# Optimization experiments

Measured on AMD Instinct MI355X. Metric: run time of the kernel, lower is better.

## Reference

```python
import jax, jax.numpy as jnp
import numpy as np

EMBED = 1024
ADIM = 1024
H = 16
HD = ADIM // H          # 64
RAY = 48                # ray_subdim
R = RAY // 3            # 16
SCALE = 1.0 / np.sqrt(HD)
NB = 768                # boundary tokens
MN = 8                  # max neighbors
FG = 6                  # face_group
L = 1024                # tokens per face
B = 12                  # b * face_group
STAGES = 4


def _apply_dray(x, d, einsum_str, inverse):
    ray = x[..., :RAY].reshape(x.shape[:-1] + (3, R))
    if inverse:
        d = jnp.swapaxes(d, -1, -2)
    ray = jnp.einsum(einsum_str, d, ray).reshape(x.shape[:-1] + (RAY,))
    return jnp.concatenate([ray, x[..., RAY:]], axis=-1)


def setup_inputs() -> dict:
    key = jax.random.key(0)
    ks = jax.random.split(key, 12)
    inp = {}
    inp['x'] = jax.random.normal(ks[0], (B, L, EMBED), dtype=jnp.float32)
    inp['qkv_w'] = jax.random.normal(ks[1], (EMBED, 3 * ADIM), dtype=jnp.float32) * 0.02
    inp['out_w'] = jax.random.normal(ks[2], (ADIM, EMBED), dtype=jnp.float32) * 0.02
    inp['out_b'] = jax.random.normal(ks[3], (EMBED,), dtype=jnp.float32) * 0.02
    inp['d_ray'] = jax.random.normal(ks[4], (STAGES, FG, L, 3, 3), dtype=jnp.float32)
    inp['boundary_face_ids'] = jax.random.randint(ks[5], (NB,), 0, FG, dtype=jnp.int32).astype(jnp.int64)
    inp['boundary_token_indices'] = jnp.arange(NB, dtype=jnp.int64)
    inp['boundary_local_indices'] = jax.random.randint(ks[6], (NB,), 0, L, dtype=jnp.int32).astype(jnp.int64)
    inp['boundary_stage_ids'] = jax.random.randint(ks[7], (NB,), 0, STAGES, dtype=jnp.int32).astype(jnp.int64)
    inp['neighbor_face_ids'] = jax.random.randint(ks[8], (NB, MN), 0, FG, dtype=jnp.int32).astype(jnp.int64)
    inp['neighbor_token_indices'] = jax.random.randint(ks[9], (NB, MN), 0, L, dtype=jnp.int32).astype(jnp.int64)
    inp['neighbor_local_indices'] = jax.random.randint(ks[10], (NB, MN), 0, L, dtype=jnp.int32).astype(jnp.int64)
    inp['neighbor_stage_ids'] = jax.random.randint(ks[11], (NB, MN), 0, STAGES, dtype=jnp.int32).astype(jnp.int64)
    inp['neighbor_mask'] = jnp.ones((NB, MN), dtype=bool)
    inp['face_group'] = FG
    return inp


def reference(x, qkv_w, out_w, out_b, d_ray,
              boundary_face_ids, boundary_token_indices, boundary_local_indices, boundary_stage_ids,
              neighbor_face_ids, neighbor_token_indices, neighbor_local_indices, neighbor_stage_ids,
              neighbor_mask, face_group):
    b = x.shape[0] // face_group
    l = x.shape[1]
    xt = x.reshape(b, face_group, l, EMBED)          # [b, FG, L, E]
    max_face, max_idx = face_group - 1, l - 1

    qf = jnp.clip(boundary_face_ids, 0, max_face)
    qi = jnp.clip(boundary_token_indices, 0, max_idx)
    valid_q = (boundary_face_ids == qf) & (boundary_token_indices == qi)

    nf = jnp.clip(neighbor_face_ids, 0, max_face)
    ni = jnp.clip(neighbor_token_indices, 0, max_idx)
    mask = neighbor_mask & (neighbor_face_ids == nf) & (neighbor_token_indices == ni)

    # gather boundary queries and neighbor keys/values
    x_q = xt[:, qf, qi, :]                            # [b, NB, E]
    x_kv = xt[:, nf, ni, :]                           # [b, NB, MN, E]
    q = (x_q @ qkv_w)[..., :ADIM]
    kv = x_kv @ qkv_w
    k = kv[..., ADIM:2 * ADIM]
    v = kv[..., 2 * ADIM:]

    nb, mn = q.shape[1], k.shape[2]
    q = q.reshape(b, nb, H, HD)
    k = k.reshape(b, nb, mn, H, HD)
    v = v.reshape(b, nb, mn, H, HD)

    d_q = d_ray[boundary_stage_ids, boundary_face_ids, boundary_local_indices]     # [NB, 3, 3]
    d_k = d_ray[neighbor_stage_ids,
                jnp.maximum(neighbor_face_ids, 0),
                jnp.maximum(neighbor_local_indices, 0)]                            # [NB, MN, 3, 3]

    q = _apply_dray(q, d_q, 'nij,bnhjr->bnhir', inverse=False)
    k = _apply_dray(k, d_k, 'nmij,bnmhjr->bnmhir', inverse=False)
    v = _apply_dray(v, d_k, 'nmij,bnmhjr->bnmhir', inverse=False)

    attn = jnp.einsum('bnhd,bnmhd->bnmh', q, k) * SCALE
    attn = jnp.where(mask[None, :, :, None], attn, -jnp.inf)
    attn = jax.nn.softmax(attn, axis=2)               # softmax over neighbors
    out = jnp.einsum('bnmh,bnmhd->bnhd', attn, v)

    out = _apply_dray(out, d_q, 'nij,bnhjr->bnhir', inverse=True)
    out = out.reshape(b, nb, ADIM) @ out_w + out_b
    out = out * valid_q[None, :, None].astype(out.dtype)

    out_full = jnp.zeros_like(xt).at[:, qf, qi, :].set(out)
    return out_full.reshape(-1, l, EMBED)
```

## Files before the change

kernel.cpp:

```cpp
#include <hip/hip_runtime.h>
#include <hip/hip_bf16.h>
#include <cstddef>

#define FG 6
#define L 1024
#define NB 768
#define MN 8
#define H 16
#define HD 64
#define ADIM 1024
#define STAGES 4
#define SCALE 0.125f

typedef __attribute__((ext_vector_type(8))) short bf16x8;
typedef __attribute__((ext_vector_type(4))) float f32x4;
typedef __attribute__((address_space(3))) short lds_short_t;
typedef const __attribute__((address_space(1))) short g_short_t;

__device__ __forceinline__ int clampi(int v, int lo, int hi) {
  return v < lo ? lo : (v > hi ? hi : v);
}

__device__ __forceinline__ short f2bf(float f) {
  __hip_bfloat16 h = __float2bfloat16(f);
  return *reinterpret_cast<short*>(&h);
}

__device__ __forceinline__ float bf2f(short s) {
  __hip_bfloat16 h = *reinterpret_cast<__hip_bfloat16*>(&s);
  return __bfloat162float(h);
}

__device__ __forceinline__ void gload16(const short* g, short* l) {
  __builtin_amdgcn_global_load_lds((g_short_t*)g, (lds_short_t*)l, 16, 0, 0);
}

__global__ __launch_bounds__(256)
void prep_kernel(const float* __restrict__ x, short* __restrict__ xb,
                 float* __restrict__ zout,
                 const float* __restrict__ qkv_w, short* __restrict__ qwT,
                 const float* __restrict__ out_w, short* __restrict__ owT) {
  const int b = blockIdx.x;
  if (b < 12288) {
    const size_t zi = ((size_t)b * 256 + threadIdx.x) * 4;
    *(float4*)(zout + zi) = (float4){0.f, 0.f, 0.f, 0.f};
    if (b >= 6144) return;
    size_t i = ((size_t)b * 256 + threadIdx.x) * 8;
    float4 a = *(const float4*)(x + i);
    float4 c = *(const float4*)(x + i + 4);
    bf16x8 v;
    v[0] = f2bf(a.x); v[1] = f2bf(a.y); v[2] = f2bf(a.z); v[3] = f2bf(a.w);
    v[4] = f2bf(c.x); v[5] = f2bf(c.y); v[6] = f2bf(c.z); v[7] = f2bf(c.w);
    *(bf16x8*)(xb + i) = v;
    return;
  }
  int t = b - 12288;
  const float* in; short* out; int N, n0, k0;
  if (t < 3072) { in = qkv_w; out = qwT; N = 3072; n0 = (t % 96) * 32; k0 = (t / 96) * 32; }
  else { t -= 3072; in = out_w; out = owT; N = 1024; n0 = (t % 32) * 32; k0 = (t / 32) * 32; }
  __shared__ float tile[32][33];
  const int tx = threadIdx.x & 31, ty = threadIdx.x >> 5;
  #pragma unroll
  for (int i = 0; i < 4; ++i)
    tile[ty + i * 8][tx] = in[(size_t)(k0 + ty + i * 8) * N + n0 + tx];
  __syncthreads();
  #pragma unroll
  for (int i = 0; i < 4; ++i)
    out[(size_t)(n0 + ty + i * 8) * 1024 + k0 + tx] =
        f2bf(tile[tx][ty + i * 8]);
}

__global__ __launch_bounds__(256)
void q_gemm64(const short* __restrict__ A, const short* __restrict__ B,
              float* __restrict__ C,
              const int* __restrict__ f_ids, const int* __restrict__ t_ids)
{
  __shared__ __align__(16) short As[4096];
  __shared__ __align__(16) short Bs[8192];

  const int tid = threadIdx.x;
  const int w = tid >> 6, lane = tid & 63;
  const int row0 = blockIdx.y * 64, col0 = blockIdx.x * 128;
  const int lr = lane & 15, lq = lane >> 4;
  const int wrow = (w >> 1) * 32, wcol = (w & 1) * 64;

  size_t asrc[2]; short* adst[2];
  #pragma unroll
  for (int c = 0; c < 2; ++c) {
    const int d = c * 256 + tid, r = d >> 3;
    const int ss = (d & 7) ^ (r & 7);
    const int rr = row0 + r;
    const int bi = rr >= NB;
    const int idx = rr - bi * NB;
    const int f = clampi(f_ids[idx], 0, FG - 1);
    const int q = clampi(t_ids[idx], 0, L - 1);
    asrc[c] = (size_t)((bi * FG + f) * L + q) * 1024 + ss * 8;
    adst[c] = As + d * 8;
  }
  size_t bsrc[4]; short* bdst[4];
  #pragma unroll
  for (int c = 0; c < 4; ++c) {
    const int d = c * 256 + tid, r = d >> 3;
    const int ss = (d & 7) ^ (r & 7);
    bsrc[c] = (size_t)(col0 + r) * 1024 + ss * 8;
    bdst[c] = Bs + d * 8;
  }

  const char* As8 = (const char*)As;
  const char* Bs8 = (const char*)Bs;
  const int swz = lr & 7;

  f32x4 acc[2][4];
  #pragma unroll
  for (int m = 0; m < 2; ++m)
    #pragma unroll
    for (int n = 0; n < 4; ++n) acc[m][n] = (f32x4){0.f, 0.f, 0.f, 0.f};

  for (int kt = 0; kt < 16; ++kt) {
    #pragma unroll
    for (int c = 0; c < 2; ++c) gload16(A + asrc[c] + kt * 64, adst[c]);
    #pragma unroll
    for (int c = 0; c < 4; ++c) gload16(B + bsrc[c] + kt * 64, bdst[c]);
    __syncthreads();
    #pragma unroll
    for (int kk = 0; kk < 2; ++kk) {
      const int so = ((kk * 4 + lq) ^ swz) << 4;
      bf16x8 av[2], bv[4];
      #pragma unroll
      for (int m = 0; m < 2; ++m)
        av[m] = *(const bf16x8*)(As8 + (wrow + m * 16 + lr) * 128 + so);
      #pragma unroll
      for (int n = 0; n < 4; ++n)
        bv[n] = *(const bf16x8*)(Bs8 + (wcol + n * 16 + lr) * 128 + so);
      #pragma unroll
      for (int m = 0; m < 2; ++m)
        #pragma unroll
        for (int n = 0; n < 4; ++n)
          acc[m][n] = __builtin_amdgcn_mfma_f32_16x16x32_bf16(
              av[m], bv[n], acc[m][n], 0, 0, 0);
    }
    __syncthreads();
  }

  #pragma unroll
  for (int m = 0; m < 2; ++m)
    #pragma unroll
    for (int j = 0; j < 4; ++j) {
      const int r = row0 + wrow + m * 16 + lq * 4 + j;
      #pragma unroll
      for (int n = 0; n < 4; ++n)
        C[(size_t)r * 1024 + col0 + wcol + n * 16 + lr] = acc[m][n][j];
    }
}


#define BAR()   do { __builtin_amdgcn_s_barrier(); __builtin_amdgcn_sched_barrier(0); } while (0)
#define LGKM(N) do { asm volatile("s_waitcnt lgkmcnt(" #N ")" ::: "memory"); __builtin_amdgcn_sched_barrier(0); } while (0)
#define VMC(N)  do { asm volatile("s_waitcnt vmcnt(" #N ")" ::: "memory"); __builtin_amdgcn_sched_barrier(0); } while (0)
#define PRIO1   __builtin_amdgcn_s_setprio(1)
#define PRIO0   __builtin_amdgcn_s_setprio(0)

#define LDA6(D, FB, KK, BUF)                                                  \
  { _Pragma("unroll")                                                         \
    for (int f_ = 0; f_ < 3; ++f_) {                                          \
      const int row_ = (2 * ((FB) + f_) + wm) * 16 + lr;                      \
      D[f_] = *(const bf16x8*)(As8 + (BUF) * 24576 + row_ * 128               \
               + ((((KK) * 4 + lq) ^ swz) << 4));                             \
    } }

#define LDB4(D, KK, BUF)                                                      \
  { _Pragma("unroll")                                                         \
    for (int g_ = 0; g_ < 4; ++g_) {                                          \
      const int row_ = wn * 64 + g_ * 16 + lr;                                \
      D[g_] = *(const bf16x8*)(Bs8 + (BUF) * 32768 + row_ * 128               \
               + ((((KK) * 4 + lq) ^ swz) << 4));                             \
    } }

#define MM6(AV, BV, FB)                                                       \
  { _Pragma("unroll")                                                         \
    for (int f_ = 0; f_ < 3; ++f_)                                            \
      _Pragma("unroll")                                                       \
      for (int g_ = 0; g_ < 4; ++g_)                                          \
        acc[(FB) + f_][g_] = __builtin_amdgcn_mfma_f32_16x16x32_bf16(         \
            AV[f_], BV[g_], acc[(FB) + f_][g_], 0, 0, 0); }

__global__ __launch_bounds__(512, 2)
void kv_gemm192(const short* __restrict__ A, const short* __restrict__ B,
                short* __restrict__ C,
                const int* __restrict__ f_ids, const int* __restrict__ t_ids)
{
  __shared__ __align__(16) short As[24576];
  __shared__ __align__(16) short Bs[32768];

  const int tid = threadIdx.x;
  const int w = tid >> 6, lane = tid & 63;
  const int wm = w >> 2, wn = w & 3;
  const int lr = lane & 15, lq = lane >> 4;
  const int row0 = blockIdx.y * 192;
  const int col0 = blockIdx.x * 256;

  const int ssrc = (((tid & 7) ^ ((tid >> 3) & 7))) * 8;

  size_t a_src[3];
  #pragma unroll
  for (int c = 0; c < 3; ++c) {
    const int rr = row0 + c * 64 + (tid >> 3);
    const int bi = rr >= NB * MN;
    const int idx = rr - bi * (NB * MN);
    const int f = clampi(f_ids[idx], 0, FG - 1);
    const int q = clampi(t_ids[idx], 0, L - 1);
    a_src[c] = (size_t)((bi * FG + f) * L + q) * 1024 + ssrc;
  }
  size_t b_src[2][2];
  #pragma unroll
  for (int h = 0; h < 2; ++h)
    #pragma unroll
    for (int i = 0; i < 2; ++i)
      b_src[h][i] = (size_t)(1024 + col0 + h * 128 + ((tid + i * 512) >> 3)) * 1024 + ssrc;

  auto stgA = [&](int c, int kt, int buf) {
    gload16(A + a_src[c] + kt * 64, As + buf * 12288 + c * 4096 + tid * 8);
  };
  auto stgB = [&](int h, int kt, int buf) {
    gload16(B + b_src[h][0] + kt * 64, Bs + buf * 16384 + h * 8192 + tid * 8);
    gload16(B + b_src[h][1] + kt * 64, Bs + buf * 16384 + h * 8192 + 4096 + tid * 8);
  };

  const char* As8 = (const char*)As;
  const char* Bs8 = (const char*)Bs;
  const int swz = lane & 7;

  f32x4 acc[6][4];
  #pragma unroll
  for (int f = 0; f < 6; ++f)
    #pragma unroll
    for (int g = 0; g < 4; ++g) acc[f][g] = (f32x4){0.f, 0.f, 0.f, 0.f};

  bf16x8 avA[3], avB[3], bv0[4], bv1[4];

  stgB(0, 0, 0); stgB(1, 0, 0); stgA(0, 0, 0); stgA(1, 0, 0); stgA(2, 0, 0);
  stgB(0, 1, 1); stgB(1, 1, 1); stgA(0, 1, 1);
  VMC(5); BAR();

  for (int I = 0; I < 7; ++I) {
    const int kA = 2 * I + 1, kB = 2 * I + 2, kC = 2 * I + 3;
    LDA6(avA, 0, 0, 0); LDB4(bv0, 0, 0); LDA6(avB, 0, 1, 0); LDB4(bv1, 1, 0);
    stgA(1, kA, 1); stgA(2, kA, 1);
    BAR(); LGKM(0); PRIO1; MM6(avA, bv0, 0); MM6(avB, bv1, 0); PRIO0; BAR();
    LDA6(avA, 3, 0, 0); LDA6(avB, 3, 1, 0);
    stgB(0, kB, 0); stgB(1, kB, 0); stgA(0, kB, 0);
    BAR(); LGKM(0); PRIO1; MM6(avA, bv0, 3); MM6(avB, bv1, 3); PRIO0; VMC(5); BAR();
    LDA6(avA, 0, 0, 1); LDB4(bv0, 0, 1); LDA6(avB, 0, 1, 1); LDB4(bv1, 1, 1);
    stgA(1, kB, 0); stgA(2, kB, 0);
    BAR(); LGKM(0); PRIO1; MM6(avA, bv0, 0); MM6(avB, bv1, 0); PRIO0; BAR();
    LDA6(avA, 3, 0, 1); LDA6(avB, 3, 1, 1);
    stgB(0, kC, 1); stgB(1, kC, 1); stgA(0, kC, 1);
    BAR(); LGKM(0); PRIO1; MM6(avA, bv0, 3); MM6(avB, bv1, 3); PRIO0; VMC(5); BAR();
  }

  {
    LDA6(avA, 0, 0, 0); LDB4(bv0, 0, 0); LDA6(avB, 0, 1, 0); LDB4(bv1, 1, 0);
    stgA(1, 15, 1); stgA(2, 15, 1);
    BAR(); LGKM(0); PRIO1; MM6(avA, bv0, 0); MM6(avB, bv1, 0); PRIO0; BAR();

    LDA6(avA, 3, 0, 0); LDA6(avB, 3, 1, 0);
    BAR(); LGKM(0); PRIO1; MM6(avA, bv0, 3); MM6(avB, bv1, 3); PRIO0; VMC(0); BAR();

    LDA6(avA, 0, 0, 1); LDB4(bv0, 0, 1); LDA6(avB, 0, 1, 1); LDB4(bv1, 1, 1);
    BAR(); LGKM(0); PRIO1; MM6(avA, bv0, 0); MM6(avB, bv1, 0); PRIO0; BAR();

    LDA6(avA, 3, 0, 1); LDA6(avB, 3, 1, 1);
    BAR(); LGKM(0); PRIO1; MM6(avA, bv0, 3); MM6(avB, bv1, 3); PRIO0;
  }

  #pragma unroll
  for (int f = 0; f < 6; ++f) {
    #pragma unroll
    for (int j = 0; j < 4; ++j) {
      const int r = row0 + (2 * f + wm) * 16 + lq * 4 + j;
      short* cp = C + (size_t)r * 2048 + col0 + wn * 64 + lr;
      #pragma unroll
      for (int g = 0; g < 4; ++g)
        cp[g * 16] = f2bf(acc[f][g][j]);
    }
  }
}

__global__ __launch_bounds__(256)
void out_gemm64(const short* __restrict__ A, const short* __restrict__ B,
                float* __restrict__ C,
                const int* __restrict__ f_ids, const int* __restrict__ t_ids,
                const float* __restrict__ bias)
{
  __shared__ __align__(16) short As[4096];
  __shared__ __align__(16) short Bs[8192];

  const int tid = threadIdx.x;
  const int w = tid >> 6, lane = tid & 63;
  const int row0 = blockIdx.y * 64, col0 = blockIdx.x * 128;
  const int lr = lane & 15, lq = lane >> 4;
  const int wrow = (w >> 1) * 32, wcol = (w & 1) * 64;

  size_t asrc[2]; short* adst[2];
  #pragma unroll
  for (int c = 0; c < 2; ++c) {
    const int d = c * 256 + tid, r = d >> 3;
    const int ss = (d & 7) ^ (r & 7);
    asrc[c] = (size_t)(row0 + r) * 1024 + ss * 8;
    adst[c] = As + d * 8;
  }
  size_t bsrc[4]; short* bdst[4];
  #pragma unroll
  for (int c = 0; c < 4; ++c) {
    const int d = c * 256 + tid, r = d >> 3;
    const int ss = (d & 7) ^ (r & 7);
    bsrc[c] = (size_t)(col0 + r) * 1024 + ss * 8;
    bdst[c] = Bs + d * 8;
  }

  const char* As8 = (const char*)As;
  const char* Bs8 = (const char*)Bs;
  const int swz = lr & 7;

  f32x4 acc[2][4];
  #pragma unroll
  for (int m = 0; m < 2; ++m)
    #pragma unroll
    for (int n = 0; n < 4; ++n) acc[m][n] = (f32x4){0.f, 0.f, 0.f, 0.f};

  for (int kt = 0; kt < 16; ++kt) {
    #pragma unroll
    for (int c = 0; c < 2; ++c) gload16(A + asrc[c] + kt * 64, adst[c]);
    #pragma unroll
    for (int c = 0; c < 4; ++c) gload16(B + bsrc[c] + kt * 64, bdst[c]);
    __syncthreads();
    #pragma unroll
    for (int kk = 0; kk < 2; ++kk) {
      const int so = ((kk * 4 + lq) ^ swz) << 4;
      bf16x8 av[2], bv[4];
      #pragma unroll
      for (int m = 0; m < 2; ++m)
        av[m] = *(const bf16x8*)(As8 + (wrow + m * 16 + lr) * 128 + so);
      #pragma unroll
      for (int n = 0; n < 4; ++n)
        bv[n] = *(const bf16x8*)(Bs8 + (wcol + n * 16 + lr) * 128 + so);
      #pragma unroll
      for (int m = 0; m < 2; ++m)
        #pragma unroll
        for (int n = 0; n < 4; ++n)
          acc[m][n] = __builtin_amdgcn_mfma_f32_16x16x32_bf16(
              av[m], bv[n], acc[m][n], 0, 0, 0);
    }
    __syncthreads();
  }

  float bb[4];
  #pragma unroll
  for (int n = 0; n < 4; ++n) bb[n] = bias[col0 + wcol + n * 16 + lr];
  #pragma unroll
  for (int m = 0; m < 2; ++m)
    #pragma unroll
    for (int j = 0; j < 4; ++j) {
      const int r  = row0 + wrow + m * 16 + lq * 4 + j;
      const int bi = r >= NB;
      const int nn = r - bi * NB;
      const int bf = f_ids[nn], bt = t_ids[nn];
      const int qf = clampi(bf, 0, FG - 1), qi = clampi(bt, 0, L - 1);
      const bool valid = (bf == qf) && (bt == qi);
      const size_t obase = ((size_t)(bi * FG + qf) * L + qi) * 1024;
      #pragma unroll
      for (int n = 0; n < 4; ++n) {
        const int col = col0 + wcol + n * 16 + lr;
        C[obase + col] = valid ? (acc[m][n][j] + bb[n]) : 0.f;
      }
    }
}

__global__ __launch_bounds__(256)
void attn_kernel2(const float* __restrict__ dray,
                  const int* __restrict__ bfid, const int* __restrict__ blid,
                  const int* __restrict__ bsid,
                  const int* __restrict__ nfid, const int* __restrict__ ntid,
                  const int* __restrict__ nlid, const int* __restrict__ nsid,
                  const int* __restrict__ nmask,
                  const float* __restrict__ qbuf,
                  const short* __restrict__ kvbuf,
                  __hip_bfloat16* __restrict__ obuf)
{
  __shared__ __align__(16) short kvlds[MN * 2048];
  __shared__ float smdq[9];
  __shared__ float smdk[MN][9];
  __shared__ int   smok[MN];

  const int bn   = blockIdx.x;
  const int n    = bn % NB;
  const int tid  = threadIdx.x;
  const int w    = tid >> 6, lane = tid & 63;

  const short* kvb = kvbuf + (size_t)bn * MN * 2048;
  #pragma unroll
  for (int j = 0; j < 8; ++j)
    gload16(kvb + (j * 256 + tid) * 8, kvlds + (j * 256 + tid) * 8);

  if (tid < 9) {
    int st = clampi(bsid[n], 0, STAGES - 1);
    int f  = clampi(bfid[n], 0, FG - 1);
    int lc = clampi(blid[n], 0, L - 1);
    smdq[tid] = dray[((size_t)(st * FG + f) * L + lc) * 9 + tid];
  } else if (tid >= 64 && tid < 136) {
    const int t = tid - 64, m = t / 9, j = t - m * 9;
    const int idx = n * MN + m;
    int nst = clampi(nsid[idx], 0, STAGES - 1);
    int nfc = clampi(nfid[idx], 0, FG - 1);
    int nlc = clampi(nlid[idx], 0, L - 1);
    smdk[m][j] = dray[((size_t)(nst * FG + nfc) * L + nlc) * 9 + j];
  } else if (tid >= 192 && tid < 192 + MN) {
    const int m = tid - 192;
    const int idx = n * MN + m;
    int nf = nfid[idx], nt = ntid[idx];
    smok[m] = (nmask[idx] != 0) && nf >= 0 && nf < FG && nt >= 0 && nt < L;
  }
  __syncthreads();

  float dq[9];
  #pragma unroll
  for (int t = 0; t < 9; ++t) dq[t] = smdq[t];

  const int rr = lane & 15;

  for (int hi = 0; hi < 4; ++hi) {
    const int h = hi * 4 + w;

    const float qraw = qbuf[(size_t)bn * ADIM + h * HD + lane];
    float x0 = __shfl(qraw, rr), x1 = __shfl(qraw, 16 + rr), x2 = __shfl(qraw, 32 + rr);
    float q0 = dq[0]*x0 + dq[1]*x1 + dq[2]*x2;
    float q1 = dq[3]*x0 + dq[4]*x1 + dq[5]*x2;
    float q2 = dq[6]*x0 + dq[7]*x1 + dq[8]*x2;
    float qd = lane < 16 ? q0 : lane < 32 ? q1 : lane < 48 ? q2 : qraw;

    float s[MN], vd[MN];
    #pragma unroll
    for (int m = 0; m < MN; ++m) {
      float dk[9];
      #pragma unroll
      for (int t = 0; t < 9; ++t) dk[t] = smdk[m][t];

      float kraw = bf2f(kvlds[m * 2048 + h * HD + lane]);
      float k0 = __shfl(kraw, rr), k1 = __shfl(kraw, 16 + rr), k2 = __shfl(kraw, 32 + rr);
      float kr0 = dk[0]*k0 + dk[1]*k1 + dk[2]*k2;
      float kr1 = dk[3]*k0 + dk[4]*k1 + dk[5]*k2;
      float kr2 = dk[6]*k0 + dk[7]*k1 + dk[8]*k2;
      float kd = lane < 16 ? kr0 : lane < 32 ? kr1 : lane < 48 ? kr2 : kraw;

      float p = qd * kd;
      #pragma unroll
      for (int off = 32; off; off >>= 1) p += __shfl_xor(p, off);
      s[m] = p;

      float vraw = bf2f(kvlds[m * 2048 + 1024 + h * HD + lane]);
      float v0 = __shfl(vraw, rr), v1 = __shfl(vraw, 16 + rr), v2 = __shfl(vraw, 32 + rr);
      float vr0 = dk[0]*v0 + dk[1]*v1 + dk[2]*v2;
      float vr1 = dk[3]*v0 + dk[4]*v1 + dk[5]*v2;
      float vr2 = dk[6]*v0 + dk[7]*v1 + dk[8]*v2;
      vd[m] = lane < 16 ? vr0 : lane < 32 ? vr1 : lane < 48 ? vr2 : vraw;
    }

    float mx = -INFINITY;
    #pragma unroll
    for (int m = 0; m < MN; ++m) {
      s[m] = smok[m] ? s[m] * SCALE : -INFINITY;
      mx = fmaxf(mx, s[m]);
    }
    float den = 0.f;
    #pragma unroll
    for (int m = 0; m < MN; ++m) { s[m] = expf(s[m] - mx); den += s[m]; }
    float inv = 1.0f / den;

    float od = 0.f;
    #pragma unroll
    for (int m = 0; m < MN; ++m) od += s[m] * vd[m];
    od *= inv;

    float y0 = __shfl(od, rr), y1 = __shfl(od, 16 + rr), y2 = __shfl(od, 32 + rr);
    float t0 = dq[0]*y0 + dq[3]*y1 + dq[6]*y2;
    float t1 = dq[1]*y0 + dq[4]*y1 + dq[7]*y2;
    float t2 = dq[2]*y0 + dq[5]*y1 + dq[8]*y2;
    float outd = lane < 16 ? t0 : lane < 32 ? t1 : lane < 48 ? t2 : od;

    obuf[(size_t)bn * ADIM + h * HD + lane] = __float2bfloat16(outd);
  }
}

extern "C" void kernel_launch(void* const* d_in, const int* in_sizes, int n_in,
                              void* d_out, int out_size, void* d_ws, size_t ws_size,
                              hipStream_t stream) {
  const float* x     = (const float*)d_in[0];
  const float* qkv_w = (const float*)d_in[1];
  const float* out_w = (const float*)d_in[2];
  const float* out_b = (const float*)d_in[3];
  const float* dray  = (const float*)d_in[4];
  const int* bfid  = (const int*)d_in[5];
  const int* btid  = (const int*)d_in[6];
  const int* blid  = (const int*)d_in[7];
  const int* bsid  = (const int*)d_in[8];
  const int* nfid  = (const int*)d_in[9];
  const int* ntid  = (const int*)d_in[10];
  const int* nlid  = (const int*)d_in[11];
  const int* nsid  = (const int*)d_in[12];
  const int* nmask = (const int*)d_in[13];

  char* ws = (char*)d_ws;
  short* xb    = (short*)(ws);
  short* qwT   = (short*)(ws + 25165824);
  short* owT   = (short*)(ws + 31457280);
  float* qbuf  = (float*)(ws + 33554432);
  short* kvbuf = (short*)(ws + 39845888);
  short* obuf  = (short*)(ws + 90177536);

  prep_kernel<<<16384, 256, 0, stream>>>(x, xb, (float*)d_out,
                                         qkv_w, qwT, out_w, owT);

  q_gemm64<<<dim3(8, 24), 256, 0, stream>>>(xb, qwT, qbuf, bfid, btid);
  kv_gemm192<<<dim3(8, 64), 512, 0, stream>>>(xb, qwT, kvbuf, nfid, ntid);
  attn_kernel2<<<1536, 256, 0, stream>>>(dray, bfid, blid, bsid,
                                         nfid, ntid, nlid, nsid, nmask,
                                         qbuf, kvbuf,
                                         (__hip_bfloat16*)obuf);
  out_gemm64<<<dim3(8, 24), 256, 0, stream>>>(obuf, owT, (float*)d_out,
                                              bfid, btid, out_b);
}
```

Measured before the change: 154.8 us.

## Fuse Q projection GEMM into KV GEMM kernel as a second pass

```diff
diff --git a/kernel.cpp b/kernel.cpp
--- a/kernel.cpp
+++ b/kernel.cpp
@@ -70,90 +70,6 @@
         f2bf(tile[tx][ty + i * 8]);
 }
 
-__global__ __launch_bounds__(256)
-void q_gemm64(const short* __restrict__ A, const short* __restrict__ B,
-              float* __restrict__ C,
-              const int* __restrict__ f_ids, const int* __restrict__ t_ids)
-{
-  __shared__ __align__(16) short As[4096];
-  __shared__ __align__(16) short Bs[8192];
-
-  const int tid = threadIdx.x;
-  const int w = tid >> 6, lane = tid & 63;
-  const int row0 = blockIdx.y * 64, col0 = blockIdx.x * 128;
-  const int lr = lane & 15, lq = lane >> 4;
-  const int wrow = (w >> 1) * 32, wcol = (w & 1) * 64;
-
-  size_t asrc[2]; short* adst[2];
-  #pragma unroll
-  for (int c = 0; c < 2; ++c) {
-    const int d = c * 256 + tid, r = d >> 3;
-    const int ss = (d & 7) ^ (r & 7);
-    const int rr = row0 + r;
-    const int bi = rr >= NB;
-    const int idx = rr - bi * NB;
-    const int f = clampi(f_ids[idx], 0, FG - 1);
-    const int q = clampi(t_ids[idx], 0, L - 1);
-    asrc[c] = (size_t)((bi * FG + f) * L + q) * 1024 + ss * 8;
-    adst[c] = As + d * 8;
-  }
-  size_t bsrc[4]; short* bdst[4];
-  #pragma unroll
-  for (int c = 0; c < 4; ++c) {
-    const int d = c * 256 + tid, r = d >> 3;
-    const int ss = (d & 7) ^ (r & 7);
-    bsrc[c] = (size_t)(col0 + r) * 1024 + ss * 8;
-    bdst[c] = Bs + d * 8;
-  }
-
-  const char* As8 = (const char*)As;
-  const char* Bs8 = (const char*)Bs;
-  const int swz = lr & 7;
-
-  f32x4 acc[2][4];
-  #pragma unroll
-  for (int m = 0; m < 2; ++m)
-    #pragma unroll
-    for (int n = 0; n < 4; ++n) acc[m][n] = (f32x4){0.f, 0.f, 0.f, 0.f};
-
-  for (int kt = 0; kt < 16; ++kt) {
-    #pragma unroll
-    for (int c = 0; c < 2; ++c) gload16(A + asrc[c] + kt * 64, adst[c]);
-    #pragma unroll
-    for (int c = 0; c < 4; ++c) gload16(B + bsrc[c] + kt * 64, bdst[c]);
-    __syncthreads();
-    #pragma unroll
-    for (int kk = 0; kk < 2; ++kk) {
-      const int so = ((kk * 4 + lq) ^ swz) << 4;
-      bf16x8 av[2], bv[4];
-      #pragma unroll
-      for (int m = 0; m < 2; ++m)
-        av[m] = *(const bf16x8*)(As8 + (wrow + m * 16 + lr) * 128 + so);
-      #pragma unroll
-      for (int n = 0; n < 4; ++n)
-        bv[n] = *(const bf16x8*)(Bs8 + (wcol + n * 16 + lr) * 128 + so);
-      #pragma unroll
-      for (int m = 0; m < 2; ++m)
-        #pragma unroll
-        for (int n = 0; n < 4; ++n)
-          acc[m][n] = __builtin_amdgcn_mfma_f32_16x16x32_bf16(
-              av[m], bv[n], acc[m][n], 0, 0, 0);
-    }
-    __syncthreads();
-  }
-
-  #pragma unroll
-  for (int m = 0; m < 2; ++m)
-    #pragma unroll
-    for (int j = 0; j < 4; ++j) {
-      const int r = row0 + wrow + m * 16 + lq * 4 + j;
-      #pragma unroll
-      for (int n = 0; n < 4; ++n)
-        C[(size_t)r * 1024 + col0 + wcol + n * 16 + lr] = acc[m][n][j];
-    }
-}
-
-
 #define BAR()   do { __builtin_amdgcn_s_barrier(); __builtin_amdgcn_sched_barrier(0); } while (0)
 #define LGKM(N) do { asm volatile("s_waitcnt lgkmcnt(" #N ")" ::: "memory"); __builtin_amdgcn_sched_barrier(0); } while (0)
 #define VMC(N)  do { asm volatile("s_waitcnt vmcnt(" #N ")" ::: "memory"); __builtin_amdgcn_sched_barrier(0); } while (0)
@@ -184,20 +100,16 @@
         acc[(FB) + f_][g_] = __builtin_amdgcn_mfma_f32_16x16x32_bf16(         \
             AV[f_], BV[g_], acc[(FB) + f_][g_], 0, 0, 0); }
 
-__global__ __launch_bounds__(512, 2)
-void kv_gemm192(const short* __restrict__ A, const short* __restrict__ B,
-                short* __restrict__ C,
-                const int* __restrict__ f_ids, const int* __restrict__ t_ids)
+__device__ __forceinline__ void gemm192_pass(
+    const short* __restrict__ A, const short* __restrict__ B,
+    int row0, int col0, int bcol0, int MROW,
+    const int* __restrict__ f_ids, const int* __restrict__ t_ids,
+    short* As, short* Bs, f32x4 (&acc)[6][4])
 {
-  __shared__ __align__(16) short As[24576];
-  __shared__ __align__(16) short Bs[32768];
-
   const int tid = threadIdx.x;
   const int w = tid >> 6, lane = tid & 63;
   const int wm = w >> 2, wn = w & 3;
   const int lr = lane & 15, lq = lane >> 4;
-  const int row0 = blockIdx.y * 192;
-  const int col0 = blockIdx.x * 256;
 
   const int ssrc = (((tid & 7) ^ ((tid >> 3) & 7))) * 8;
 
@@ -205,8 +117,8 @@
   #pragma unroll
   for (int c = 0; c < 3; ++c) {
     const int rr = row0 + c * 64 + (tid >> 3);
-    const int bi = rr >= NB * MN;
-    const int idx = rr - bi * (NB * MN);
+    const int bi = rr >= MROW;
+    const int idx = rr - bi * MROW;
     const int f = clampi(f_ids[idx], 0, FG - 1);
     const int q = clampi(t_ids[idx], 0, L - 1);
     a_src[c] = (size_t)((bi * FG + f) * L + q) * 1024 + ssrc;
@@ -216,7 +128,7 @@
   for (int h = 0; h < 2; ++h)
     #pragma unroll
     for (int i = 0; i < 2; ++i)
-      b_src[h][i] = (size_t)(1024 + col0 + h * 128 + ((tid + i * 512) >> 3)) * 1024 + ssrc;
+      b_src[h][i] = (size_t)(bcol0 + col0 + h * 128 + ((tid + i * 512) >> 3)) * 1024 + ssrc;
 
   auto stgA = [&](int c, int kt, int buf) {
     gload16(A + a_src[c] + kt * 64, As + buf * 12288 + c * 4096 + tid * 8);
@@ -230,7 +142,6 @@
   const char* Bs8 = (const char*)Bs;
   const int swz = lane & 7;
 
-  f32x4 acc[6][4];
   #pragma unroll
   for (int f = 0; f < 6; ++f)
     #pragma unroll
@@ -272,16 +183,54 @@
     LDA6(avA, 3, 0, 1); LDA6(avB, 3, 1, 1);
     BAR(); LGKM(0); PRIO1; MM6(avA, bv0, 3); MM6(avB, bv1, 3); PRIO0;
   }
-
-  #pragma unroll
-  for (int f = 0; f < 6; ++f) {
-    #pragma unroll
-    for (int j = 0; j < 4; ++j) {
-      const int r = row0 + (2 * f + wm) * 16 + lq * 4 + j;
-      short* cp = C + (size_t)r * 2048 + col0 + wn * 64 + lr;
-      #pragma unroll
-      for (int g = 0; g < 4; ++g)
-        cp[g * 16] = f2bf(acc[f][g][j]);
+}
+
+__global__ __launch_bounds__(512, 2)
+void qkv_gemm192(const short* __restrict__ A, const short* __restrict__ B,
+                 short* __restrict__ Ckv, float* __restrict__ Cq,
+                 const int* __restrict__ nfid, const int* __restrict__ ntid,
+                 const int* __restrict__ bfid, const int* __restrict__ btid)
+{
+  __shared__ __align__(16) short As[24576];
+  __shared__ __align__(16) short Bs[32768];
+
+  const int tid = threadIdx.x;
+  const int w = tid >> 6, lane = tid & 63;
+  const int wm = w >> 2, wn = w & 3;
+  const int lr = lane & 15, lq = lane >> 4;
+
+  f32x4 acc[6][4];
+
+  {
+    const int row0 = blockIdx.y * 192, col0 = blockIdx.x * 256;
+    gemm192_pass(A, B, row0, col0, 1024, NB * MN, nfid, ntid, As, Bs, acc);
+    #pragma unroll
+    for (int f = 0; f < 6; ++f) {
+      #pragma unroll
+      for (int j = 0; j < 4; ++j) {
+        const int r = row0 + (2 * f + wm) * 16 + lq * 4 + j;
+        short* cp = Ckv + (size_t)r * 2048 + col0 + wn * 64 + lr;
+        #pragma unroll
+        for (int g = 0; g < 4; ++g)
+          cp[g * 16] = f2bf(acc[f][g][j]);
+      }
+    }
+  }
+
+  if (blockIdx.y < 4) {
+    BAR();
+    const int row0 = blockIdx.x * 192, col0 = blockIdx.y * 256;
+    gemm192_pass(A, B, row0, col0, 0, NB, bfid, btid, As, Bs, acc);
+    #pragma unroll
+    for (int f = 0; f < 6; ++f) {
+      #pragma unroll
+      for (int j = 0; j < 4; ++j) {
+        const int r = row0 + (2 * f + wm) * 16 + lq * 4 + j;
+        float* cp = Cq + (size_t)r * 1024 + col0 + wn * 64 + lr;
+        #pragma unroll
+        for (int g = 0; g < 4; ++g)
+          cp[g * 16] = acc[f][g][j];
+      }
     }
   }
 }
@@ -520,8 +469,8 @@
   prep_kernel<<<16384, 256, 0, stream>>>(x, xb, (float*)d_out,
                                          qkv_w, qwT, out_w, owT);
 
-  q_gemm64<<<dim3(8, 24), 256, 0, stream>>>(xb, qwT, qbuf, bfid, btid);
-  kv_gemm192<<<dim3(8, 64), 512, 0, stream>>>(xb, qwT, kvbuf, nfid, ntid);
+  qkv_gemm192<<<dim3(8, 64), 512, 0, stream>>>(xb, qwT, kvbuf, qbuf,
+                                               nfid, ntid, bfid, btid);
   attn_kernel2<<<1536, 256, 0, stream>>>(dray, bfid, blid, bsid,
                                          nfid, ntid, nlid, nsid, nmask,
                                          qbuf, kvbuf,
```

After: 160.9 us. 1.04x slower.

## Shrink KV gather-GEMM tile to 192x128 with remapped block order for higher occupancy

Applied to the files above, without the earlier changes.

```diff
diff --git a/kernel.cpp b/kernel.cpp
--- a/kernel.cpp
+++ b/kernel.cpp
@@ -153,55 +153,51 @@
     }
 }
 
-
 #define BAR()   do { __builtin_amdgcn_s_barrier(); __builtin_amdgcn_sched_barrier(0); } while (0)
 #define LGKM(N) do { asm volatile("s_waitcnt lgkmcnt(" #N ")" ::: "memory"); __builtin_amdgcn_sched_barrier(0); } while (0)
 #define VMC(N)  do { asm volatile("s_waitcnt vmcnt(" #N ")" ::: "memory"); __builtin_amdgcn_sched_barrier(0); } while (0)
 #define PRIO1   __builtin_amdgcn_s_setprio(1)
 #define PRIO0   __builtin_amdgcn_s_setprio(0)
 
-#define LDA6(D, FB, KK, BUF)                                                  \
+#define LDAF(D, FR, KK, BUF)                                                  \
+  D = *(const bf16x8*)(As8 + (BUF) * 24576 +                                  \
+        ((4 * (FR) + wm) * 16 + lr) * 128 + ((((KK) * 4 + lq) ^ swz) << 4));
+
+#define LDBF(D, KK, BUF)                                                      \
   { _Pragma("unroll")                                                         \
-    for (int f_ = 0; f_ < 3; ++f_) {                                          \
-      const int row_ = (2 * ((FB) + f_) + wm) * 16 + lr;                      \
-      D[f_] = *(const bf16x8*)(As8 + (BUF) * 24576 + row_ * 128               \
-               + ((((KK) * 4 + lq) ^ swz) << 4));                             \
-    } }
-
-#define LDB4(D, KK, BUF)                                                      \
+    for (int g_ = 0; g_ < 4; ++g_)                                            \
+      D[g_] = *(const bf16x8*)(Bs8 + (BUF) * 16384 +                          \
+                (wn * 64 + g_ * 16 + lr) * 128 +                              \
+                ((((KK) * 4 + lq) ^ swz) << 4)); }
+
+#define MMF(AV, BV, FR)                                                       \
   { _Pragma("unroll")                                                         \
-    for (int g_ = 0; g_ < 4; ++g_) {                                          \
-      const int row_ = wn * 64 + g_ * 16 + lr;                                \
-      D[g_] = *(const bf16x8*)(Bs8 + (BUF) * 32768 + row_ * 128               \
-               + ((((KK) * 4 + lq) ^ swz) << 4));                             \
-    } }
-
-#define MM6(AV, BV, FB)                                                       \
-  { _Pragma("unroll")                                                         \
-    for (int f_ = 0; f_ < 3; ++f_)                                            \
-      _Pragma("unroll")                                                       \
-      for (int g_ = 0; g_ < 4; ++g_)                                          \
-        acc[(FB) + f_][g_] = __builtin_amdgcn_mfma_f32_16x16x32_bf16(         \
-            AV[f_], BV[g_], acc[(FB) + f_][g_], 0, 0, 0); }
-
-__global__ __launch_bounds__(512, 2)
+    for (int g_ = 0; g_ < 4; ++g_)                                            \
+      acc[FR][g_] = __builtin_amdgcn_mfma_f32_16x16x32_bf16(                  \
+          AV, BV[g_], acc[FR][g_], 0, 0, 0); }
+
+__global__ __launch_bounds__(512, 4)
 void kv_gemm192(const short* __restrict__ A, const short* __restrict__ B,
                 short* __restrict__ C,
                 const int* __restrict__ f_ids, const int* __restrict__ t_ids)
 {
   __shared__ __align__(16) short As[24576];
-  __shared__ __align__(16) short Bs[32768];
+  __shared__ __align__(16) short Bs[16384];
 
   const int tid = threadIdx.x;
   const int w = tid >> 6, lane = tid & 63;
-  const int wm = w >> 2, wn = w & 3;
+  const int wm = w >> 1;
+  const int wn = w & 1;
   const int lr = lane & 15, lq = lane >> 4;
-  const int row0 = blockIdx.y * 192;
-  const int col0 = blockIdx.x * 256;
+
+  const int bid = blockIdx.y * 16 + blockIdx.x;
+  const int sid = (bid & 7) * 128 + (bid >> 3);
+  const int row0 = (sid >> 4) * 192;
+  const int col0 = (sid & 15) * 128;
 
   const int ssrc = (((tid & 7) ^ ((tid >> 3) & 7))) * 8;
 
-  size_t a_src[3];
+  int a_src[3];
   #pragma unroll
   for (int c = 0; c < 3; ++c) {
     const int rr = row0 + c * 64 + (tid >> 3);
@@ -209,75 +205,92 @@
     const int idx = rr - bi * (NB * MN);
     const int f = clampi(f_ids[idx], 0, FG - 1);
     const int q = clampi(t_ids[idx], 0, L - 1);
-    a_src[c] = (size_t)((bi * FG + f) * L + q) * 1024 + ssrc;
-  }
-  size_t b_src[2][2];
-  #pragma unroll
-  for (int h = 0; h < 2; ++h)
-    #pragma unroll
-    for (int i = 0; i < 2; ++i)
-      b_src[h][i] = (size_t)(1024 + col0 + h * 128 + ((tid + i * 512) >> 3)) * 1024 + ssrc;
+    a_src[c] = ((bi * FG + f) * L + q) * 1024 + ssrc;
+  }
+  int b_src[2];
+  #pragma unroll
+  for (int i = 0; i < 2; ++i)
+    b_src[i] = (1024 + col0 + (tid >> 3) + i * 64) * 1024 + ssrc;
 
   auto stgA = [&](int c, int kt, int buf) {
     gload16(A + a_src[c] + kt * 64, As + buf * 12288 + c * 4096 + tid * 8);
   };
-  auto stgB = [&](int h, int kt, int buf) {
-    gload16(B + b_src[h][0] + kt * 64, Bs + buf * 16384 + h * 8192 + tid * 8);
-    gload16(B + b_src[h][1] + kt * 64, Bs + buf * 16384 + h * 8192 + 4096 + tid * 8);
+  auto stgB = [&](int kt, int buf) {
+    gload16(B + b_src[0] + kt * 64, Bs + buf * 8192 + tid * 8);
+    gload16(B + b_src[1] + kt * 64, Bs + buf * 8192 + 4096 + tid * 8);
   };
 
   const char* As8 = (const char*)As;
   const char* Bs8 = (const char*)Bs;
   const int swz = lane & 7;
 
-  f32x4 acc[6][4];
-  #pragma unroll
-  for (int f = 0; f < 6; ++f)
+  f32x4 acc[3][4];
+  #pragma unroll
+  for (int f = 0; f < 3; ++f)
     #pragma unroll
     for (int g = 0; g < 4; ++g) acc[f][g] = (f32x4){0.f, 0.f, 0.f, 0.f};
 
-  bf16x8 avA[3], avB[3], bv0[4], bv1[4];
-
-  stgB(0, 0, 0); stgB(1, 0, 0); stgA(0, 0, 0); stgA(1, 0, 0); stgA(2, 0, 0);
-  stgB(0, 1, 1); stgB(1, 1, 1); stgA(0, 1, 1);
-  VMC(5); BAR();
+  bf16x8 a00, a10, a01, a11, a20, a21, bv0[4], bv1[4];
+
+  stgB(0, 0); stgA(0, 0, 0); stgA(1, 0, 0); stgA(2, 0, 0);
+  stgB(1, 1); stgA(0, 1, 1);
+  VMC(3); BAR();
 
   for (int I = 0; I < 7; ++I) {
     const int kA = 2 * I + 1, kB = 2 * I + 2, kC = 2 * I + 3;
-    LDA6(avA, 0, 0, 0); LDB4(bv0, 0, 0); LDA6(avB, 0, 1, 0); LDB4(bv1, 1, 0);
+    LDAF(a00, 0, 0, 0); LDAF(a10, 1, 0, 0); LDBF(bv0, 0, 0);
+    LDAF(a01, 0, 1, 0); LDAF(a11, 1, 1, 0); LDBF(bv1, 1, 0);
     stgA(1, kA, 1); stgA(2, kA, 1);
-    BAR(); LGKM(0); PRIO1; MM6(avA, bv0, 0); MM6(avB, bv1, 0); PRIO0; BAR();
-    LDA6(avA, 3, 0, 0); LDA6(avB, 3, 1, 0);
-    stgB(0, kB, 0); stgB(1, kB, 0); stgA(0, kB, 0);
-    BAR(); LGKM(0); PRIO1; MM6(avA, bv0, 3); MM6(avB, bv1, 3); PRIO0; VMC(5); BAR();
-    LDA6(avA, 0, 0, 1); LDB4(bv0, 0, 1); LDA6(avB, 0, 1, 1); LDB4(bv1, 1, 1);
+    BAR(); LGKM(0);
+    PRIO1; MMF(a00, bv0, 0); MMF(a10, bv0, 1); MMF(a01, bv1, 0); MMF(a11, bv1, 1); PRIO0;
+    BAR();
+    LDAF(a20, 2, 0, 0); LDAF(a21, 2, 1, 0);
+    stgB(kB, 0); stgA(0, kB, 0);
+    BAR(); LGKM(0);
+    PRIO1; MMF(a20, bv0, 2); MMF(a21, bv1, 2); PRIO0;
+    VMC(3); BAR();
+    LDAF(a00, 0, 0, 1); LDAF(a10, 1, 0, 1); LDBF(bv0, 0, 1);
+    LDAF(a01, 0, 1, 1); LDAF(a11, 1, 1, 1); LDBF(bv1, 1, 1);
     stgA(1, kB, 0); stgA(2, kB, 0);
-    BAR(); LGKM(0); PRIO1; MM6(avA, bv0, 0); MM6(avB, bv1, 0); PRIO0; BAR();
-    LDA6(avA, 3, 0, 1); LDA6(avB, 3, 1, 1);
-    stgB(0, kC, 1); stgB(1, kC, 1); stgA(0, kC, 1);
-    BAR(); LGKM(0); PRIO1; MM6(avA, bv0, 3); MM6(avB, bv1, 3); PRIO0; VMC(5); BAR();
+    BAR(); LGKM(0);
+    PRIO1; MMF(a00, bv0, 0); MMF(a10, bv0, 1); MMF(a01, bv1, 0); MMF(a11, bv1, 1); PRIO0;
+    BAR();
+    LDAF(a20, 2, 0, 1); LDAF(a21, 2, 1, 1);
+    stgB(kC, 1); stgA(0, kC, 1);
+    BAR(); LGKM(0);
+    PRIO1; MMF(a20, bv0, 2); MMF(a21, bv1, 2); PRIO0;
+    VMC(3); BAR();
   }
 
   {
-    LDA6(avA, 0, 0, 0); LDB4(bv0, 0, 0); LDA6(avB, 0, 1, 0); LDB4(bv1, 1, 0);
+    LDAF(a00, 0, 0, 0); LDAF(a10, 1, 0, 0); LDBF(bv0, 0, 0);
+    LDAF(a01, 0, 1, 0); LDAF(a11, 1, 1, 0); LDBF(bv1, 1, 0);
     stgA(1, 15, 1); stgA(2, 15, 1);
-    BAR(); LGKM(0); PRIO1; MM6(avA, bv0, 0); MM6(avB, bv1, 0); PRIO0; BAR();
-
-    LDA6(avA, 3, 0, 0); LDA6(avB, 3, 1, 0);
-    BAR(); LGKM(0); PRIO1; MM6(avA, bv0, 3); MM6(avB, bv1, 3); PRIO0; VMC(0); BAR();
-
-    LDA6(avA, 0, 0, 1); LDB4(bv0, 0, 1); LDA6(avB, 0, 1, 1); LDB4(bv1, 1, 1);
-    BAR(); LGKM(0); PRIO1; MM6(avA, bv0, 0); MM6(avB, bv1, 0); PRIO0; BAR();
-
-    LDA6(avA, 3, 0, 1); LDA6(avB, 3, 1, 1);
-    BAR(); LGKM(0); PRIO1; MM6(avA, bv0, 3); MM6(avB, bv1, 3); PRIO0;
-  }
-
-  #pragma unroll
-  for (int f = 0; f < 6; ++f) {
+    BAR(); LGKM(0);
+    PRIO1; MMF(a00, bv0, 0); MMF(a10, bv0, 1); MMF(a01, bv1, 0); MMF(a11, bv1, 1); PRIO0;
+    BAR();
+
+    LDAF(a20, 2, 0, 0); LDAF(a21, 2, 1, 0);
+    BAR(); LGKM(0);
+    PRIO1; MMF(a20, bv0, 2); MMF(a21, bv1, 2); PRIO0;
+    VMC(0); BAR();
+
+    LDAF(a00, 0, 0, 1); LDAF(a10, 1, 0, 1); LDBF(bv0, 0, 1);
+    LDAF(a01, 0, 1, 1); LDAF(a11, 1, 1, 1); LDBF(bv1, 1, 1);
+    BAR(); LGKM(0);
+    PRIO1; MMF(a00, bv0, 0); MMF(a10, bv0, 1); MMF(a01, bv1, 0); MMF(a11, bv1, 1); PRIO0;
+    BAR();
+
+    LDAF(a20, 2, 0, 1); LDAF(a21, 2, 1, 1);
+    BAR(); LGKM(0);
+    PRIO1; MMF(a20, bv0, 2); MMF(a21, bv1, 2); PRIO0;
+  }
+
+  #pragma unroll
+  for (int f = 0; f < 3; ++f) {
     #pragma unroll
     for (int j = 0; j < 4; ++j) {
-      const int r = row0 + (2 * f + wm) * 16 + lq * 4 + j;
+      const int r = row0 + (4 * f + wm) * 16 + lq * 4 + j;
       short* cp = C + (size_t)r * 2048 + col0 + wn * 64 + lr;
       #pragma unroll
       for (int g = 0; g < 4; ++g)
@@ -521,7 +534,7 @@
                                          qkv_w, qwT, out_w, owT);
 
   q_gemm64<<<dim3(8, 24), 256, 0, stream>>>(xb, qwT, qbuf, bfid, btid);
-  kv_gemm192<<<dim3(8, 64), 512, 0, stream>>>(xb, qwT, kvbuf, nfid, ntid);
+  kv_gemm192<<<dim3(16, 64), 512, 0, stream>>>(xb, qwT, kvbuf, nfid, ntid);
   attn_kernel2<<<1536, 256, 0, stream>>>(dray, bfid, blid, bsid,
                                          nfid, ntid, nlid, nsid, nmask,
                                          qbuf, kvbuf,
```

After: 148.3 us (median of 2 runs). 4.2% less time.
